# Performance work log

Measured on AMD Instinct MI355X. Metric: run time of the kernel, lower is better.

The kernel has to match this reference:

```python
import jax, jax.numpy as jnp
import numpy as np

HEADS = 8
DIM_HEAD = 64
NUM_LANDMARKS = 256
PINV_ITERS = 6
SCALE = DIM_HEAD ** -0.5
KERNEL = 33
PAD = KERNEL // 2


def moore_penrose_iter_pinv(x, iters=PINV_ITERS):
    # x: [b, h, m, m]
    abs_x = jnp.abs(x)
    col = abs_x.sum(axis=-1)
    row = abs_x.sum(axis=-2)
    # global max over all batch/head entries, as in the torch code
    z = jnp.swapaxes(x, -1, -2) / (jnp.max(col) * jnp.max(row))
    I = jnp.eye(x.shape[-1], dtype=x.dtype)
    for _ in range(iters):
        xz = x @ z
        z = 0.25 * z @ (13.0 * I - xz @ (15.0 * I - xz @ (7.0 * I - xz)))
    return z


def setup_inputs() -> dict:
    key = jax.random.key(0)
    k1, k2, k3, k4 = jax.random.split(key, 4)
    b, n, dim = 4, 4096, 512
    inner = HEADS * DIM_HEAD
    return {
        "x": jax.random.normal(k1, (b, n, dim), dtype=jnp.float32),
        "w_qkv": jax.random.normal(k2, (dim, 3 * inner), dtype=jnp.float32) * 0.02,
        "w_out": jax.random.normal(k3, (inner, dim), dtype=jnp.float32) * 0.02,
        "b_out": jnp.zeros((dim,), dtype=jnp.float32),
        "conv_w": jax.random.normal(k4, (HEADS, 1, KERNEL, 1), dtype=jnp.float32) * 0.1,
    }


def reference(x, w_qkv, w_out, b_out, conv_w):
    b, n, dim = x.shape
    h, m = HEADS, NUM_LANDMARKS
    # n is a multiple of m, so the original's left-padding branch is a no-op
    qkv = x @ w_qkv  # [b, n, 3*h*d]
    q, k, v = jnp.split(qkv, 3, axis=-1)

    def split_heads(t):
        return t.reshape(b, n, h, DIM_HEAD).transpose(0, 2, 1, 3)  # [b,h,n,d]

    q, k, v = split_heads(q), split_heads(k), split_heads(v)
    q = q * SCALE

    l = n // m  # landmark group size
    q_l = q.reshape(b, h, m, l, DIM_HEAD).mean(axis=3)  # [b,h,m,d]
    k_l = k.reshape(b, h, m, l, DIM_HEAD).mean(axis=3)

    sim1 = jnp.einsum("bhid,bhjd->bhij", q, k_l)   # [b,h,n,m]
    sim2 = jnp.einsum("bhid,bhjd->bhij", q_l, k_l)  # [b,h,m,m]
    sim3 = jnp.einsum("bhid,bhjd->bhij", q_l, k)   # [b,h,m,n]

    attn1 = jax.nn.softmax(sim1, axis=-1)
    attn2 = jax.nn.softmax(sim2, axis=-1)
    attn3 = jax.nn.softmax(sim3, axis=-1)

    attn2_inv = moore_penrose_iter_pinv(attn2, PINV_ITERS)
    out = attn1 @ (attn2_inv @ (attn3 @ v))  # [b,h,n,d]

    # residual depthwise conv along sequence dim (kernel 33x1, groups=heads)
    res = jax.lax.conv_general_dilated(
        v, conv_w,
        window_strides=(1, 1),
        padding=((PAD, PAD), (0, 0)),
        dimension_numbers=("NCHW", "OIHW", "NCHW"),
        feature_group_count=h,
    )
    out = out + res

    out = out.transpose(0, 2, 1, 3).reshape(b, n, h * DIM_HEAD)
    out = out @ w_out + b_out
    return out  # out[:, -n:] is identity since no padding was applied
```

## Files before the change

### kernel.cpp

```cpp
#include <hip/hip_runtime.h>
#include <math.h>


#define QKV_STRIDE 262144
#define LM_STRIDE 16384
#define MM_STRIDE 65536

typedef float f32x4 __attribute__((ext_vector_type(4)));
typedef short bf8 __attribute__((ext_vector_type(8)));
typedef short s4v __attribute__((ext_vector_type(4)));

__device__ __forceinline__ unsigned short f2bf_(float f) {
  unsigned u = __float_as_uint(f);
  u += 0x7FFFu + ((u >> 16) & 1u);
  return (unsigned short)(u >> 16);
}
__device__ __forceinline__ float bf2f_(unsigned short h) {
  return __uint_as_float(((unsigned)h) << 16);
}

__device__ __forceinline__ void gl16(const short* g, short* l) {
  __builtin_amdgcn_global_load_lds(
      (const __attribute__((address_space(1))) unsigned int*)g,
      (__attribute__((address_space(3))) unsigned int*)l, 16, 0, 0);
}

__global__ __launch_bounds__(256) void zero_scal(float* scal) {
  if (threadIdx.x < 2) scal[threadIdx.x] = 0.0f;
}

__global__ __launch_bounds__(256) void x_to_bf16(const float* __restrict__ x,
                                                 short* __restrict__ xb) {
  const int g = blockIdx.x * 256 + threadIdx.x;
  const float4* xp = (const float4*)x;
#pragma unroll
  for (int u = 0; u < 4; ++u) {
    const size_t i4 = (size_t)u * 524288 + g;
    float4 v = xp[i4];
    s4v o;
    o[0] = (short)f2bf_(v.x); o[1] = (short)f2bf_(v.y);
    o[2] = (short)f2bf_(v.z); o[3] = (short)f2bf_(v.w);
    *(s4v*)&xb[i4 * 4] = o;
  }
}

__global__ __launch_bounds__(256) void transpose_bf16(const float* __restrict__ src,
                                                      short* __restrict__ dst,
                                                      int R, int C) {
  __shared__ float T[32][33];
  const int t = threadIdx.x;
  const int c0 = blockIdx.x * 32, r0 = blockIdx.y * 32;
  const int tr = t >> 3, tc = (t & 7) << 2;
  float4 vsrc = *(const float4*)&src[(size_t)(r0 + tr) * C + c0 + tc];
  T[tr][tc + 0] = vsrc.x; T[tr][tc + 1] = vsrc.y;
  T[tr][tc + 2] = vsrc.z; T[tr][tc + 3] = vsrc.w;
  __syncthreads();
  s4v o;
  o[0] = (short)f2bf_(T[tc + 0][tr]);
  o[1] = (short)f2bf_(T[tc + 1][tr]);
  o[2] = (short)f2bf_(T[tc + 2][tr]);
  o[3] = (short)f2bf_(T[tc + 3][tr]);
  *(s4v*)&dst[(size_t)(c0 + tr) * R + r0 + tc] = o;
}

__global__ __launch_bounds__(256) void gemm_qkv_mfma(const short* __restrict__ xb,
                                                     const short* __restrict__ wT,
                                                     short* __restrict__ qb16,
                                                     short* __restrict__ kb16,
                                                     short* __restrict__ vT16) {
  __shared__ short SMEM[17408];
  short* As = SMEM;
  short* Bs = SMEM + 4096;
  const int tid = threadIdx.x;
  const int lane = tid & 63, w = tid >> 6;
  const int wr = w >> 1, wc = w & 1;
  const int bid = (blockIdx.x & 7) * 192 + (blockIdx.x >> 3);
  const int bn = bid % 12, bm = bid / 12;
  const int gm0 = bm * 128, gn0 = bn * 128;
  const int mA0 = (tid >> 6) * 16 + (tid & 15), kA0 = ((tid >> 4) & 3) * 8;
  const int s1 = tid + 256;
  const int mA1 = (s1 >> 6) * 16 + (s1 & 15), kA1 = ((s1 >> 4) & 3) * 8;
  const short* srcA0 = &xb[(size_t)(gm0 + mA0) * 512 + kA0];
  const short* srcA1 = &xb[(size_t)(gm0 + mA1) * 512 + kA1];
  const short* srcB0 = &wT[(size_t)(gn0 + mA0) * 512 + kA0];
  const short* srcB1 = &wT[(size_t)(gn0 + mA1) * 512 + kA1];
  short* dA0 = &As[w * 512];
  short* dA1 = &As[2048 + w * 512];
  short* dB0 = &Bs[w * 512];
  short* dB1 = &Bs[2048 + w * 512];
  f32x4 acc[4][4];
#pragma unroll
  for (int i = 0; i < 4; ++i)
#pragma unroll
    for (int j = 0; j < 4; ++j) acc[i][j] = (f32x4){0.f, 0.f, 0.f, 0.f};
  for (int kt = 0; kt < 16; ++kt) {
    const int k0 = kt * 32;
    __syncthreads();
    gl16(srcA0 + k0, dA0);
    gl16(srcA1 + k0, dA1);
    gl16(srcB0 + k0, dB0);
    gl16(srcB1 + k0, dB1);
    __syncthreads();
    bf8 af[4], bf[4];
#pragma unroll
    for (int i = 0; i < 4; ++i) {
      af[i] = *(const bf8*)&As[((wr * 4 + i) * 64 + lane) * 8];
      bf[i] = *(const bf8*)&Bs[((wc * 4 + i) * 64 + lane) * 8];
    }
#pragma unroll
    for (int i = 0; i < 4; ++i)
#pragma unroll
      for (int j = 0; j < 4; ++j)
        acc[i][j] = __builtin_amdgcn_mfma_f32_16x16x32_bf16(af[i], bf[j], acc[i][j], 0, 0, 0);
  }
  const int which = bn >> 2;
  const int qd = lane >> 4, c = lane & 15;
  if (which < 2) {
    short* dst = which == 0 ? qb16 : kb16;
    const float scale = which == 0 ? 0.125f : 1.0f;
#pragma unroll
    for (int i = 0; i < 4; ++i)
#pragma unroll
      for (int j = 0; j < 4; ++j) {
        const int col = gn0 + wc * 64 + j * 16 + c;
        const int head = (col >> 6) & 7, dd = col & 63;
#pragma unroll
        for (int r = 0; r < 4; ++r) {
          const int row = gm0 + wr * 64 + i * 16 + qd * 4 + r;
          const int b = row >> 12, seq = row & 4095;
          dst[(size_t)(b * 8 + head) * QKV_STRIDE + seq * 64 + dd] =
              (short)f2bf_(acc[i][j][r] * scale);
        }
      }
  } else {
    __syncthreads();
#pragma unroll
    for (int i = 0; i < 4; ++i)
#pragma unroll
      for (int j = 0; j < 4; ++j) {
        const int colL = wc * 64 + j * 16 + c;
#pragma unroll
        for (int r = 0; r < 4; ++r) {
          const int rowL = wr * 64 + i * 16 + qd * 4 + r;
          SMEM[colL * 136 + rowL] = (short)f2bf_(acc[i][j][r]);
        }
      }
    __syncthreads();
    const int b = gm0 >> 12, seq0 = gm0 & 4095;
    const int dcol = tid >> 1, half = tid & 1;
    const int col = gn0 + dcol;
    const int head = (col >> 6) & 7, d = col & 63;
    const short* src = &SMEM[dcol * 136 + half * 64];
    short* dstp = &vT16[(size_t)(b * 8 + head) * QKV_STRIDE + (size_t)d * 4096 +
                        seq0 + half * 64];
#pragma unroll
    for (int u = 0; u < 16; ++u) *(s4v*)&dstp[u * 4] = *(const s4v*)&src[u * 4];
  }
}

__global__ __launch_bounds__(256) void lmk_mean(const short* __restrict__ qb16,
                                                const short* __restrict__ kb16,
                                                float* __restrict__ ql,
                                                float* __restrict__ kl,
                                                short* __restrict__ klb16) {
  const int g = blockIdx.x * 256 + threadIdx.x;
  const int dd = g & 63, mi = (g >> 6) & 255, bh = g >> 14;
  const size_t base = (size_t)bh * QKV_STRIDE + mi * 1024 + dd;
  float sq = 0.f, sk = 0.f;
#pragma unroll
  for (int jj = 0; jj < 16; ++jj) {
    sq += bf2f_((unsigned short)qb16[base + jj * 64]);
    sk += bf2f_((unsigned short)kb16[base + jj * 64]);
  }
  const float qv = sq * 0.0625f, kv = sk * 0.0625f;
  ql[g] = qv;
  kl[g] = kv;
  klb16[g] = (short)f2bf_(kv);
}

__global__ __launch_bounds__(256) void sim2_softmax(const float* __restrict__ ql,
                                                    const float* __restrict__ kl,
                                                    short* __restrict__ x2hi,
                                                    short* __restrict__ x2lo) {
  const int blk = blockIdx.x;
  const int bh = blk >> 4, rg = blk & 15;
  __shared__ float Qs[16][64];
  __shared__ float Ks[64][68];
  __shared__ float S[16][257];
  __shared__ float red[16][17];
  __shared__ float rowinv[16];
  const int tid = threadIdx.x;
  const int r = tid >> 4, jc = tid & 15;
#pragma unroll
  for (int u = 0; u < 4; ++u) {
    int t2 = tid + u * 256;
    Qs[t2 >> 6][t2 & 63] =
        ql[(size_t)bh * LM_STRIDE + (rg * 16 + (t2 >> 6)) * 64 + (t2 & 63)];
  }
  for (int c = 0; c < 4; ++c) {
    __syncthreads();
#pragma unroll
    for (int u = 0; u < 4; ++u) {
      int t4 = tid + u * 256;
      int row = t4 >> 4, c4 = (t4 & 15) << 2;
      *(float4*)&Ks[row][c4] =
          *(const float4*)&kl[(size_t)bh * LM_STRIDE + (c * 64 + row) * 64 + c4];
    }
    __syncthreads();
#pragma unroll
    for (int s = 0; s < 4; ++s) {
      const int jj = jc + (s << 4);
      float acc = 0.f;
#pragma unroll
      for (int k4 = 0; k4 < 16; ++k4) {
        const float4 a = *(const float4*)&Qs[r][k4 << 2];
        const float4 bb = *(const float4*)&Ks[jj][k4 << 2];
        acc += a.x * bb.x + a.y * bb.y + a.z * bb.z + a.w * bb.w;
      }
      S[r][(c << 6) + jj] = acc;
    }
  }
  __syncthreads();
  float pm = -3.0e38f;
#pragma unroll
  for (int u = 0; u < 16; ++u) pm = fmaxf(pm, S[r][jc + (u << 4)]);
  red[r][jc] = pm;
  __syncthreads();
  float m = red[r][0];
#pragma unroll
  for (int u = 1; u < 16; ++u) m = fmaxf(m, red[r][u]);
  __syncthreads();
  float ps = 0.f;
#pragma unroll
  for (int u = 0; u < 16; ++u) {
    const int j = jc + (u << 4);
    const float e = __expf(S[r][j] - m);
    S[r][j] = e;
    ps += e;
  }
  red[r][jc] = ps;
  __syncthreads();
  if (jc == 0) {
    float sum = 0.f;
#pragma unroll
    for (int u = 0; u < 16; ++u) sum += red[r][u];
    rowinv[r] = 1.0f / sum;
  }
  __syncthreads();
  for (int idx = tid; idx < 4096; idx += 256) {
    const int rr = idx >> 8, j = idx & 255;
    const float v = S[rr][j] * rowinv[rr];
    const unsigned short h = f2bf_(v);
    const size_t off = (size_t)bh * MM_STRIDE + (rg * 16 + rr) * 256 + j;
    x2hi[off] = (short)h;
    x2lo[off] = (short)f2bf_(v - bf2f_(h));
  }
}

__global__ __launch_bounds__(256) void colrow_max(const short* __restrict__ x2hi,
                                                  const short* __restrict__ x2lo,
                                                  float* __restrict__ scal) {
  const int bh = blockIdx.x;
  const int tid = threadIdx.x;
  const size_t b0 = (size_t)bh * MM_STRIDE;
  float cs = 0.f, rs = 0.f;
  for (int j = 0; j < 256; ++j) {
    const size_t o = b0 + (size_t)tid * 256 + j;
    cs += fabsf(bf2f_((unsigned short)x2hi[o]) + bf2f_((unsigned short)x2lo[o]));
  }
  for (int i = 0; i < 256; ++i) {
    const size_t o = b0 + (size_t)i * 256 + tid;
    rs += fabsf(bf2f_((unsigned short)x2hi[o]) + bf2f_((unsigned short)x2lo[o]));
  }
  __shared__ float rc[256], rr[256];
  rc[tid] = cs; rr[tid] = rs;
  __syncthreads();
  for (int st = 128; st > 0; st >>= 1) {
    if (tid < st) {
      rc[tid] = fmaxf(rc[tid], rc[tid + st]);
      rr[tid] = fmaxf(rr[tid], rr[tid + st]);
    }
    __syncthreads();
  }
  if (tid == 0) {
    atomicMax((int*)&scal[0], __float_as_int(rc[0]));
    atomicMax((int*)&scal[1], __float_as_int(rr[0]));
  }
}

__global__ __launch_bounds__(256) void tscale2(const short* __restrict__ x2hi,
                                               const short* __restrict__ x2lo,
                                               const float* __restrict__ scal,
                                               short* __restrict__ zBhi,
                                               short* __restrict__ zBlo,
                                               short* __restrict__ zAhi,
                                               short* __restrict__ zAlo,
                                               float* __restrict__ zf) {
  const int g = blockIdx.x * 256 + threadIdx.x;
  const int j = g & 255, i = (g >> 8) & 255, bh = g >> 16;
  const float inv = 1.0f / (scal[0] * scal[1]);
  const float val = (bf2f_((unsigned short)x2hi[g]) +
                     bf2f_((unsigned short)x2lo[g])) * inv;
  const unsigned short h = f2bf_(val);
  const unsigned short lo = f2bf_(val - bf2f_(h));
  zBhi[g] = (short)h;
  zBlo[g] = (short)lo;
  const size_t tg = (size_t)bh * MM_STRIDE + (size_t)j * 256 + i;
  zAhi[tg] = (short)h;
  zAlo[tg] = (short)lo;
  zf[tg] = val;
}

__global__ __launch_bounds__(256) void pinv_mfma(const short* __restrict__ Ahi_g,
                                                 const short* __restrict__ Alo_g,
                                                 const short* __restrict__ Bhi_g,
                                                 const short* __restrict__ Blo_g,
                                                 const float* __restrict__ Ef,
                                                 float* __restrict__ Cf,
                                                 short* __restrict__ Chi,
                                                 short* __restrict__ Clo,
                                                 short* __restrict__ CThi,
                                                 short* __restrict__ CTlo,
                                                 float alpha, float beta,
                                                 int wantCf, int wantChl,
                                                 int wantT) {
  __shared__ short Ah[2048], Al[2048], Bh[2048], Bl[2048];
  __shared__ float Tbuf[64 * 68];
  const int tid = threadIdx.x;
  const int lane = tid & 63, w = tid >> 6;
  const int bid = blockIdx.x;
  const int xcd = bid & 7, y = bid >> 3;
  const int t16 = y & 15, bgrp = y >> 4;
  const int batch = bgrp * 8 + xcd;
  const int tm = t16 >> 2, tn = t16 & 3;
  const size_t bb = (size_t)batch * MM_STRIDE;
  const int ml = (tid >> 6) * 16 + (tid & 15), koff = ((tid >> 4) & 3) * 8;
  const short* sAh = Ahi_g + bb + (size_t)(tm * 64 + ml) * 256 + koff;
  const short* sAl = Alo_g + bb + (size_t)(tm * 64 + ml) * 256 + koff;
  const short* sBh = Bhi_g + bb + (size_t)(tn * 64 + ml) * 256 + koff;
  const short* sBl = Blo_g + bb + (size_t)(tn * 64 + ml) * 256 + koff;
  short* dAh = &Ah[w * 512];
  short* dAl = &Al[w * 512];
  short* dBh = &Bh[w * 512];
  short* dBl = &Bl[w * 512];
  f32x4 acc[4];
#pragma unroll
  for (int j = 0; j < 4; ++j) acc[j] = (f32x4){0.f, 0.f, 0.f, 0.f};
  for (int kt = 0; kt < 8; ++kt) {
    const int k0 = kt * 32;
    __syncthreads();
    gl16(sAh + k0, dAh);
    gl16(sAl + k0, dAl);
    gl16(sBh + k0, dBh);
    gl16(sBl + k0, dBl);
    __syncthreads();
    bf8 ah = *(const bf8*)&Ah[(w * 64 + lane) * 8];
    bf8 al = *(const bf8*)&Al[(w * 64 + lane) * 8];
#pragma unroll
    for (int j = 0; j < 4; ++j) {
      bf8 bh = *(const bf8*)&Bh[(j * 64 + lane) * 8];
      bf8 bl = *(const bf8*)&Bl[(j * 64 + lane) * 8];
      acc[j] = __builtin_amdgcn_mfma_f32_16x16x32_bf16(ah, bh, acc[j], 0, 0, 0);
      acc[j] = __builtin_amdgcn_mfma_f32_16x16x32_bf16(ah, bl, acc[j], 0, 0, 0);
      acc[j] = __builtin_amdgcn_mfma_f32_16x16x32_bf16(al, bh, acc[j], 0, 0, 0);
    }
  }
  const int qd = lane >> 4, c = lane & 15;
  float vals[4][4];
#pragma unroll
  for (int j = 0; j < 4; ++j) {
    const int col = tn * 64 + j * 16 + c;
#pragma unroll
    for (int r = 0; r < 4; ++r) {
      const int row = tm * 64 + w * 16 + qd * 4 + r;
      const size_t off = bb + (size_t)row * 256 + col;
      float e = 0.f;
      if (alpha != 0.0f) e = alpha * Ef[off];
      const float vv = e + beta * acc[j][r];
      vals[j][r] = vv;
      if (wantCf) Cf[off] = vv;
      if (wantChl) {
        const unsigned short h = f2bf_(vv);
        Chi[off] = (short)h;
        Clo[off] = (short)f2bf_(vv - bf2f_(h));
      }
    }
  }
  if (wantT) {
    __syncthreads();
#pragma unroll
    for (int j = 0; j < 4; ++j)
#pragma unroll
      for (int r = 0; r < 4; ++r)
        Tbuf[(j * 16 + c) * 68 + w * 16 + qd * 4 + r] = vals[j][r];
    __syncthreads();
    const int ctr = tid >> 2, seg = (tid & 3) * 16;
#pragma unroll
    for (int u = 0; u < 4; ++u) {
      float4 o = *(const float4*)&Tbuf[ctr * 68 + seg + u * 4];
      s4v hi, lo;
      unsigned short h;
      h = f2bf_(o.x); hi[0] = (short)h; lo[0] = (short)f2bf_(o.x - bf2f_(h));
      h = f2bf_(o.y); hi[1] = (short)h; lo[1] = (short)f2bf_(o.y - bf2f_(h));
      h = f2bf_(o.z); hi[2] = (short)h; lo[2] = (short)f2bf_(o.z - bf2f_(h));
      h = f2bf_(o.w); hi[3] = (short)h; lo[3] = (short)f2bf_(o.w - bf2f_(h));
      const size_t off = bb + (size_t)(tn * 64 + ctr) * 256 + tm * 64 + seg + u * 4;
      *(s4v*)&CThi[off] = hi;
      *(s4v*)&CTlo[off] = lo;
    }
  }
}

__global__ __launch_bounds__(256) void attn3_flash(const float* __restrict__ ql,
                                                   const short* __restrict__ kb16,
                                                   const short* __restrict__ vT16,
                                                   float* __restrict__ opart,
                                                   float* __restrict__ mpart,
                                                   float* __restrict__ lpart) {
  const int kc = blockIdx.x;
  const int rt = blockIdx.y;
  const int bh = blockIdx.z;
  __shared__ short Pa[4][4096];
  const int tid = threadIdx.x, lane = tid & 63, w = tid >> 6;
  const int qd = lane >> 4, c = lane & 15;
  const int rw = rt * 64 + w * 16;
  const float* qlp = ql + (size_t)bh * LM_STRIDE;
  const short* kp = kb16 + (size_t)bh * QKV_STRIDE;
  const short* vp = vT16 + (size_t)bh * QKV_STRIDE;
  short* Pw = &Pa[w][0];
  bf8 af[2];
#pragma unroll
  for (int st = 0; st < 2; ++st) {
    float4 x0 = *(const float4*)&qlp[(size_t)(rw + c) * 64 + st * 32 + qd * 8];
    float4 x1 = *(const float4*)&qlp[(size_t)(rw + c) * 64 + st * 32 + qd * 8 + 4];
    bf8 r;
    r[0] = (short)f2bf_(x0.x); r[1] = (short)f2bf_(x0.y);
    r[2] = (short)f2bf_(x0.z); r[3] = (short)f2bf_(x0.w);
    r[4] = (short)f2bf_(x1.x); r[5] = (short)f2bf_(x1.y);
    r[6] = (short)f2bf_(x1.z); r[7] = (short)f2bf_(x1.w);
    af[st] = r;
  }
  float m[4], l[4];
#pragma unroll
  for (int r = 0; r < 4; ++r) { m[r] = -3.0e38f; l[r] = 0.f; }
  f32x4 accO[4];
#pragma unroll
  for (int nb = 0; nb < 4; ++nb) accO[nb] = (f32x4){0.f, 0.f, 0.f, 0.f};
  for (int it = 0; it < 4; ++it) {
    const int kb0 = kc * 1024 + it * 256;
    f32x4 acc[16];
#pragma unroll
    for (int j = 0; j < 16; ++j) acc[j] = (f32x4){0.f, 0.f, 0.f, 0.f};
#pragma unroll
    for (int st = 0; st < 2; ++st)
#pragma unroll
      for (int j = 0; j < 16; ++j) {
        bf8 bfk = *(const bf8*)&kp[(size_t)(kb0 + j * 16 + c) * 64 + st * 32 + qd * 8];
        acc[j] = __builtin_amdgcn_mfma_f32_16x16x32_bf16(af[st], bfk, acc[j], 0, 0, 0);
      }
#pragma unroll
    for (int r = 0; r < 4; ++r) {
      float mx = acc[0][r];
#pragma unroll
      for (int j = 1; j < 16; ++j) mx = fmaxf(mx, acc[j][r]);
      mx = fmaxf(mx, __shfl_xor(mx, 1));
      mx = fmaxf(mx, __shfl_xor(mx, 2));
      mx = fmaxf(mx, __shfl_xor(mx, 4));
      mx = fmaxf(mx, __shfl_xor(mx, 8));
      const float mN = fmaxf(m[r], mx);
      const float a = __expf(m[r] - mN);
      m[r] = mN;
      l[r] *= a;
#pragma unroll
      for (int nb = 0; nb < 4; ++nb) accO[nb][r] *= a;
      float s = 0.f;
#pragma unroll
      for (int j = 0; j < 16; ++j) {
        const float e = __expf(acc[j][r] - mN);
        acc[j][r] = e;
        s += e;
      }
      s += __shfl_xor(s, 1);
      s += __shfl_xor(s, 2);
      s += __shfl_xor(s, 4);
      s += __shfl_xor(s, 8);
      l[r] += s;
    }
#pragma unroll
    for (int j = 0; j < 16; ++j) {
      const int kcol = j * 16 + c;
      const int kb8 = kcol >> 5;
      const int la_base = 16 * ((kcol >> 3) & 3);
      const int j8 = kcol & 7;
#pragma unroll
      for (int r = 0; r < 4; ++r) {
        const int rl = qd * 4 + r;
        Pw[(kb8 * 64 + la_base + rl) * 8 + j8] = (short)f2bf_(acc[j][r]);
      }
    }
#pragma unroll
    for (int kbk = 0; kbk < 8; ++kbk) {
      bf8 ap = *(const bf8*)&Pw[(kbk * 64 + lane) * 8];
#pragma unroll
      for (int nb = 0; nb < 4; ++nb) {
        bf8 bv = *(const bf8*)&vp[(size_t)(nb * 16 + c) * 4096 + kb0 + kbk * 32 + qd * 8];
        accO[nb] = __builtin_amdgcn_mfma_f32_16x16x32_bf16(ap, bv, accO[nb], 0, 0, 0);
      }
    }
  }
  const size_t ob = ((size_t)kc * 32 + bh) * 256 + rt * 64;
#pragma unroll
  for (int nb = 0; nb < 4; ++nb)
#pragma unroll
    for (int r = 0; r < 4; ++r)
      opart[(ob + w * 16 + qd * 4 + r) * 64 + nb * 16 + c] = accO[nb][r];
  if (c == 0) {
#pragma unroll
    for (int r = 0; r < 4; ++r) {
      mpart[ob + w * 16 + qd * 4 + r] = m[r];
      lpart[ob + w * 16 + qd * 4 + r] = l[r];
    }
  }
}

__global__ __launch_bounds__(256) void attn3_merge(const float* __restrict__ opart,
                                                   const float* __restrict__ mpart,
                                                   const float* __restrict__ lpart,
                                                   short* __restrict__ avth,
                                                   short* __restrict__ avtl) {
  const int g = blockIdx.x * 256 + threadIdx.x;
  const int d = g & 63;
  const int idx = g >> 6;
  const int bh = idx >> 8, row = idx & 255;
  const float m0 = mpart[idx], m1 = mpart[8192 + idx],
              m2 = mpart[16384 + idx], m3 = mpart[24576 + idx];
  const float mx = fmaxf(fmaxf(m0, m1), fmaxf(m2, m3));
  const float w0 = __expf(m0 - mx), w1 = __expf(m1 - mx),
              w2 = __expf(m2 - mx), w3 = __expf(m3 - mx);
  const float l = lpart[idx] * w0 + lpart[8192 + idx] * w1 +
                  lpart[16384 + idx] * w2 + lpart[24576 + idx] * w3;
  const float o = opart[(size_t)idx * 64 + d] * w0 +
                  opart[524288 + (size_t)idx * 64 + d] * w1 +
                  opart[1048576 + (size_t)idx * 64 + d] * w2 +
                  opart[1572864 + (size_t)idx * 64 + d] * w3;
  const float val = o / l;
  const unsigned short h = f2bf_(val);
  const size_t o2 = ((size_t)bh * 64 + d) * 256 + row;
  avth[o2] = (short)h;
  avtl[o2] = (short)f2bf_(val - bf2f_(h));
}

__global__ __launch_bounds__(256) void zav_mfma(const short* __restrict__ zAhi,
                                                const short* __restrict__ zAlo,
                                                const short* __restrict__ avth,
                                                const short* __restrict__ avtl,
                                                short* __restrict__ w2tb16) {
  __shared__ short Tb[64 * 68];
  const int rt = blockIdx.x;
  const int bh = blockIdx.y;
  const int tid = threadIdx.x, lane = tid & 63, w = tid >> 6;
  const int qd = lane >> 4, c = lane & 15;
  const size_t zoff = (size_t)bh * MM_STRIDE + (size_t)(rt * 64 + w * 16 + c) * 256;
  const short* zh = zAhi + zoff;
  const short* zl = zAlo + zoff;
  const short* ahp = avth + (size_t)bh * LM_STRIDE;
  const short* alp = avtl + (size_t)bh * LM_STRIDE;
  f32x4 acc[4];
#pragma unroll
  for (int j = 0; j < 4; ++j) acc[j] = (f32x4){0.f, 0.f, 0.f, 0.f};
  for (int kt = 0; kt < 8; ++kt) {
    const int k0 = kt * 32 + qd * 8;
    bf8 ah = *(const bf8*)&zh[k0];
    bf8 al = *(const bf8*)&zl[k0];
#pragma unroll
    for (int j = 0; j < 4; ++j) {
      bf8 bhj = *(const bf8*)&ahp[(size_t)(j * 16 + c) * 256 + k0];
      bf8 blj = *(const bf8*)&alp[(size_t)(j * 16 + c) * 256 + k0];
      acc[j] = __builtin_amdgcn_mfma_f32_16x16x32_bf16(ah, bhj, acc[j], 0, 0, 0);
      acc[j] = __builtin_amdgcn_mfma_f32_16x16x32_bf16(ah, blj, acc[j], 0, 0, 0);
      acc[j] = __builtin_amdgcn_mfma_f32_16x16x32_bf16(al, bhj, acc[j], 0, 0, 0);
    }
  }
#pragma unroll
  for (int j = 0; j < 4; ++j)
#pragma unroll
    for (int r = 0; r < 4; ++r)
      Tb[(j * 16 + c) * 68 + w * 16 + qd * 4 + r] = (short)f2bf_(acc[j][r]);
  __syncthreads();
  const int col = tid >> 2, rs = (tid & 3) * 16;
  short* dst = &w2tb16[(size_t)bh * LM_STRIDE + (size_t)col * 256 + rt * 64 + rs];
  const short* srcp = &Tb[col * 68 + rs];
#pragma unroll
  for (int u = 0; u < 4; ++u) *(s4v*)&dst[u * 4] = *(const s4v*)&srcp[u * 4];
}

__global__ __launch_bounds__(256) void attn1_conv_mfma(const short* __restrict__ qb16,
                                                       const short* __restrict__ klb16,
                                                       const short* __restrict__ w2tb16,
                                                       const short* __restrict__ vT16,
                                                       const float* __restrict__ cw,
                                                       short* __restrict__ ohb16) {
  __shared__ short Pa[16384];
  __shared__ float redM[4][64], redS[4][64];
  __shared__ float rowM[64], rowI[64];
  __shared__ float cwS[33];
  const int tid = threadIdx.x;
  const int lane = tid & 63, w = tid >> 6;
  const int qd = lane >> 4, c = lane & 15;
  const int r0 = blockIdx.x * 64;
  const int bh = blockIdx.y;
  const short* qp = qb16 + (size_t)bh * QKV_STRIDE;
  const short* klp = klb16 + (size_t)bh * LM_STRIDE;
  const short* w2p = w2tb16 + (size_t)bh * LM_STRIDE;
  const short* vp = vT16 + (size_t)bh * QKV_STRIDE;

  if (tid < 33) cwS[tid] = cw[(bh & 7) * 33 + tid];

  f32x4 acc[4][4];
#pragma unroll
  for (int i = 0; i < 4; ++i)
#pragma unroll
    for (int j = 0; j < 4; ++j) acc[i][j] = (f32x4){0.f, 0.f, 0.f, 0.f};
#pragma unroll
  for (int st = 0; st < 2; ++st) {
    const int k0 = st * 32 + qd * 8;
    bf8 af[4], bf[4];
#pragma unroll
    for (int i = 0; i < 4; ++i) {
      af[i] = *(const bf8*)&qp[(size_t)(r0 + i * 16 + c) * 64 + k0];
      bf[i] = *(const bf8*)&klp[(size_t)(w * 64 + i * 16 + c) * 64 + k0];
    }
#pragma unroll
    for (int i = 0; i < 4; ++i)
#pragma unroll
      for (int j = 0; j < 4; ++j)
        acc[i][j] = __builtin_amdgcn_mfma_f32_16x16x32_bf16(af[i], bf[j], acc[i][j], 0, 0, 0);
  }
#pragma unroll
  for (int i = 0; i < 4; ++i)
#pragma unroll
    for (int r = 0; r < 4; ++r) {
      float m0 = fmaxf(fmaxf(acc[i][0][r], acc[i][1][r]),
                       fmaxf(acc[i][2][r], acc[i][3][r]));
      m0 = fmaxf(m0, __shfl_xor(m0, 1));
      m0 = fmaxf(m0, __shfl_xor(m0, 2));
      m0 = fmaxf(m0, __shfl_xor(m0, 4));
      m0 = fmaxf(m0, __shfl_xor(m0, 8));
      if (c == 0) redM[w][i * 16 + qd * 4 + r] = m0;
    }
  __syncthreads();
  if (tid < 64)
    rowM[tid] = fmaxf(fmaxf(redM[0][tid], redM[1][tid]),
                      fmaxf(redM[2][tid], redM[3][tid]));
  __syncthreads();
#pragma unroll
  for (int i = 0; i < 4; ++i)
#pragma unroll
    for (int r = 0; r < 4; ++r) {
      const float mrow = rowM[i * 16 + qd * 4 + r];
      float s = 0.f;
#pragma unroll
      for (int j = 0; j < 4; ++j) {
        const float e = __expf(acc[i][j][r] - mrow);
        acc[i][j][r] = e;
        s += e;
      }
      s += __shfl_xor(s, 1);
      s += __shfl_xor(s, 2);
      s += __shfl_xor(s, 4);
      s += __shfl_xor(s, 8);
      if (c == 0) redS[w][i * 16 + qd * 4 + r] = s;
    }
  __syncthreads();
  if (tid < 64)
    rowI[tid] = 1.0f / (redS[0][tid] + redS[1][tid] + redS[2][tid] + redS[3][tid]);
  __syncthreads();
#pragma unroll
  for (int i = 0; i < 4; ++i)
#pragma unroll
    for (int r = 0; r < 4; ++r) {
      const int row = i * 16 + qd * 4 + r;
      const float inv = rowI[row];
#pragma unroll
      for (int j = 0; j < 4; ++j) {
        const int col = w * 64 + j * 16 + c;
        const short val = (short)f2bf_(acc[i][j][r] * inv);
        const int kb = col >> 5;
        const int lane2 = (row & 15) + 16 * ((col >> 3) & 3);
        Pa[((kb * 4 + i) * 64 + lane2) * 8 + (col & 7)] = val;
      }
    }
  __syncthreads();
  f32x4 accO[4];
#pragma unroll
  for (int nb = 0; nb < 4; ++nb) accO[nb] = (f32x4){0.f, 0.f, 0.f, 0.f};
  for (int kb = 0; kb < 8; ++kb) {
    bf8 ap = *(const bf8*)&Pa[((kb * 4 + w) * 64 + lane) * 8];
#pragma unroll
    for (int nb = 0; nb < 4; ++nb) {
      bf8 bfr = *(const bf8*)&w2p[(size_t)(nb * 16 + c) * 256 + kb * 32 + qd * 8];
      accO[nb] = __builtin_amdgcn_mfma_f32_16x16x32_bf16(ap, bfr, accO[nb], 0, 0, 0);
    }
  }
  {
    bf8 ba[3];
    const int rl = w * 16 + (lane & 15);
#pragma unroll
    for (int kb = 0; kb < 3; ++kb) {
#pragma unroll
      for (int e = 0; e < 8; ++e) {
        const int kk = kb * 32 + qd * 8 + e;
        const int t = kk - rl;
        const int s = r0 - 16 + kk;
        const float bv = (t >= 0 && t < 33 && s >= 0 && s < 4096) ? cwS[t] : 0.f;
        ba[kb][e] = (short)f2bf_(bv);
      }
    }
#pragma unroll
    for (int kb = 0; kb < 3; ++kb) {
      int s0 = r0 - 16 + kb * 32 + qd * 8;
      s0 = s0 < 0 ? 0 : (s0 > 4088 ? 4088 : s0);
#pragma unroll
      for (int nb = 0; nb < 4; ++nb) {
        bf8 bv = *(const bf8*)&vp[(size_t)(nb * 16 + c) * 4096 + s0];
        accO[nb] = __builtin_amdgcn_mfma_f32_16x16x32_bf16(ba[kb], bv, accO[nb], 0, 0, 0);
      }
    }
  }
  short* ohp = (short*)ohb16 + (size_t)bh * QKV_STRIDE;
#pragma unroll
  for (int nb = 0; nb < 4; ++nb)
#pragma unroll
    for (int r = 0; r < 4; ++r) {
      const int row = r0 + w * 16 + qd * 4 + r;
      ohp[(size_t)row * 64 + nb * 16 + c] = (short)f2bf_(accO[nb][r]);
    }
}

__global__ __launch_bounds__(256) void gemm_out_mfma(const short* __restrict__ ohb16,
                                                     const short* __restrict__ wT,
                                                     const float* __restrict__ bias,
                                                     float* __restrict__ out) {
  __shared__ short As[4096];
  __shared__ short Bs[4096];
  const int tid = threadIdx.x;
  const int lane = tid & 63, w = tid >> 6;
  const int wr = w >> 1, wc = w & 1;
  const int bid = (blockIdx.x & 7) * 64 + (blockIdx.x >> 3);
  const int bn = bid & 3, bm = bid >> 2;
  const int gm0 = bm * 128, gn0 = bn * 128;
  const int mA0 = (tid >> 6) * 16 + (tid & 15), kA0 = ((tid >> 4) & 3) * 8;
  const int s1 = tid + 256;
  const int mA1 = (s1 >> 6) * 16 + (s1 & 15), kA1 = ((s1 >> 4) & 3) * 8;
  const int b0r = (gm0 + mA0) >> 12, seq0 = (gm0 + mA0) & 4095;
  const int b1r = (gm0 + mA1) >> 12, seq1 = (gm0 + mA1) & 4095;
  short* dA0 = &As[w * 512];
  short* dA1 = &As[2048 + w * 512];
  short* dB0 = &Bs[w * 512];
  short* dB1 = &Bs[2048 + w * 512];
  f32x4 acc[4][4];
#pragma unroll
  for (int i = 0; i < 4; ++i)
#pragma unroll
    for (int j = 0; j < 4; ++j) acc[i][j] = (f32x4){0.f, 0.f, 0.f, 0.f};
  for (int kt = 0; kt < 16; ++kt) {
    const int ka = kt * 32 + kA0, kb = kt * 32 + kA1;
    __syncthreads();
    gl16(&ohb16[(size_t)(b0r * 8 + (ka >> 6)) * QKV_STRIDE + (size_t)seq0 * 64 + (ka & 63)], dA0);
    gl16(&ohb16[(size_t)(b1r * 8 + (kb >> 6)) * QKV_STRIDE + (size_t)seq1 * 64 + (kb & 63)], dA1);
    gl16(&wT[(size_t)(gn0 + mA0) * 512 + ka], dB0);
    gl16(&wT[(size_t)(gn0 + mA1) * 512 + kb], dB1);
    __syncthreads();
    bf8 af[4], bfr[4];
#pragma unroll
    for (int i = 0; i < 4; ++i) {
      af[i] = *(const bf8*)&As[((wr * 4 + i) * 64 + lane) * 8];
      bfr[i] = *(const bf8*)&Bs[((wc * 4 + i) * 64 + lane) * 8];
    }
#pragma unroll
    for (int i = 0; i < 4; ++i)
#pragma unroll
      for (int j = 0; j < 4; ++j)
        acc[i][j] = __builtin_amdgcn_mfma_f32_16x16x32_bf16(af[i], bfr[j], acc[i][j], 0, 0, 0);
  }
  const int qd = lane >> 4, c = lane & 15;
#pragma unroll
  for (int i = 0; i < 4; ++i)
#pragma unroll
    for (int j = 0; j < 4; ++j) {
      const int col = gn0 + wc * 64 + j * 16 + c;
      const float bval = bias[col];
#pragma unroll
      for (int r = 0; r < 4; ++r) {
        const int row = gm0 + wr * 64 + i * 16 + qd * 4 + r;
        out[(size_t)row * 512 + col] = acc[i][j][r] + bval;
      }
    }
}

extern "C" void kernel_launch(void* const* d_in, const int* in_sizes, int n_in,
                              void* d_out, int out_size, void* d_ws, size_t ws_size,
                              hipStream_t stream) {
  const float* x    = (const float*)d_in[0];
  const float* wqkv = (const float*)d_in[1];
  const float* wout = (const float*)d_in[2];
  const float* bout = (const float*)d_in[3];
  const float* cw   = (const float*)d_in[4];
  float* out = (float*)d_out;

  float* w = (float*)d_ws;
  short* qb16   = (short*)(w);
  short* kb16   = (short*)(w + 4194304);
  short* vT16   = (short*)(w + 8388608);
  short* xb16   = (short*)(w + 12582912);
  float* z0f    = w + 12582912;
  float* z1f    = w + 14680064;
  float* opart  = w + 12582912;
  short* ohb16  = (short*)(w + 12582912);
  float* ql     = w + 16777216;
  float* kl     = w + 17301504;
  short* klb16  = (short*)(w + 17825792);
  short* x2hi   = (short*)(w + 18087936);
  short* x2lo   = (short*)(w + 19136512);
  float* xzf    = w + 20185088;
  short* xzAhi  = (short*)(w + 22282240);
  short* xzAlo  = (short*)(w + 23330816);
  short* xzBhi  = (short*)(w + 24379392);
  short* xzBlo  = (short*)(w + 25427968);
  short* u1Bhi  = (short*)(w + 26476544);
  short* u1Blo  = (short*)(w + 27525120);
  short* z0Ahi  = (short*)(w + 28573696);
  short* z0Alo  = (short*)(w + 29622272);
  short* z0Bhi  = (short*)(w + 30670848);
  short* z0Blo  = (short*)(w + 31719424);
  short* z1Ahi  = (short*)(w + 32768000);
  short* z1Alo  = (short*)(w + 33816576);
  short* z1Bhi  = (short*)(w + 34865152);
  short* z1Blo  = (short*)(w + 35913728);
  float* scal   = w + 36962304;
  short* wqkvT  = (short*)(w + 36962368);
  short* woutT  = (short*)(w + 37355584);
  short* avth   = (short*)(w + 20185088);
  short* avtl   = (short*)(w + 20447232);
  short* w2tb16 = (short*)(w + 20709376);
  float* mpart  = w + 26476544;
  float* lpart  = w + 26509312;

  zero_scal<<<1, 64, 0, stream>>>(scal);
  transpose_bf16<<<dim3(48, 16), 256, 0, stream>>>(wqkv, wqkvT, 512, 1536);
  transpose_bf16<<<dim3(16, 16), 256, 0, stream>>>(wout, woutT, 512, 512);
  x_to_bf16<<<2048, 256, 0, stream>>>(x, xb16);
  gemm_qkv_mfma<<<1536, 256, 0, stream>>>(xb16, wqkvT, qb16, kb16, vT16);
  lmk_mean<<<2048, 256, 0, stream>>>(qb16, kb16, ql, kl, klb16);
  sim2_softmax<<<512, 256, 0, stream>>>(ql, kl, x2hi, x2lo);
  colrow_max<<<32, 256, 0, stream>>>(x2hi, x2lo, scal);
  tscale2<<<8192, 256, 0, stream>>>(x2hi, x2lo, scal, z0Bhi, z0Blo, z0Ahi, z0Alo, z0f);

  float *zcf = z0f, *znf = z1f;
  short *zAh = z0Ahi, *zAl = z0Alo, *zBh = z0Bhi, *zBl = z0Blo;
  short *nAh = z1Ahi, *nAl = z1Alo, *nBh = z1Bhi, *nBl = z1Blo;
  for (int it = 0; it < 6; ++it) {
    pinv_mfma<<<512, 256, 0, stream>>>(x2hi, x2lo, zBh, zBl, xzf,
                                       xzf, xzAhi, xzAlo, xzBhi, xzBlo,
                                       0.f, 1.f, 1, 1, 1);
    pinv_mfma<<<512, 256, 0, stream>>>(xzAhi, xzAlo, xzBhi, xzBlo, xzf,
                                       znf, u1Bhi, u1Blo, u1Bhi, u1Blo,
                                       7.f, -1.f, 0, 0, 1);
    pinv_mfma<<<512, 256, 0, stream>>>(xzAhi, xzAlo, u1Bhi, u1Blo, xzf,
                                       znf, xzBhi, xzBlo, xzBhi, xzBlo,
                                       15.f, -1.f, 0, 0, 1);
    pinv_mfma<<<512, 256, 0, stream>>>(zAh, zAl, xzBhi, xzBlo, zcf,
                                       znf, nAh, nAl, nBh, nBl,
                                       3.25f, -0.25f, 1, 1, 1);
    float* tf = zcf; zcf = znf; znf = tf;
    short* t;
    t = zAh; zAh = nAh; nAh = t;  t = zAl; zAl = nAl; nAl = t;
    t = zBh; zBh = nBh; nBh = t;  t = zBl; zBl = nBl; nBl = t;
  }

  attn3_flash<<<dim3(4, 4, 32), 256, 0, stream>>>(ql, kb16, vT16, opart, mpart, lpart);
  attn3_merge<<<2048, 256, 0, stream>>>(opart, mpart, lpart, avth, avtl);
  zav_mfma<<<dim3(4, 32), 256, 0, stream>>>(zAh, zAl, avth, avtl, w2tb16);
  attn1_conv_mfma<<<dim3(64, 32), 256, 0, stream>>>(qb16, klb16, w2tb16, vT16, cw, ohb16);
  gemm_out_mfma<<<512, 256, 0, stream>>>(ohb16, woutT, bout, out);
}
```

Before: 801.4 us.

## Give each wave full softmax rows in attn1 kernel, remap blocks to XCDs, skip unused pinv outputs

```diff
diff --git a/kernel.cpp b/kernel.cpp
--- a/kernel.cpp
+++ b/kernel.cpp
@@ -137,7 +137,7 @@
 #pragma unroll
     for (int i = 0; i < 4; ++i)
 #pragma unroll
-      for (int j = 0; j < 4; ++j) {
+    for (int j = 0; j < 4; ++j) {
         const int colL = wc * 64 + j * 16 + c;
 #pragma unroll
         for (int r = 0; r < 4; ++r) {
@@ -600,125 +600,101 @@
                                                        const short* __restrict__ vT16,
                                                        const float* __restrict__ cw,
                                                        short* __restrict__ ohb16) {
-  __shared__ short Pa[16384];
-  __shared__ float redM[4][64], redS[4][64];
-  __shared__ float rowM[64], rowI[64];
+  __shared__ short Pa[4][4096];
   __shared__ float cwS[33];
-  const int tid = threadIdx.x;
-  const int lane = tid & 63, w = tid >> 6;
+  const int tid = threadIdx.x, lane = tid & 63, w = tid >> 6;
   const int qd = lane >> 4, c = lane & 15;
-  const int r0 = blockIdx.x * 64;
-  const int bh = blockIdx.y;
+  const int lin = blockIdx.x;
+  const int xcd = lin & 7;
+  const int idx = lin >> 3;
+  const int bh = xcd * 4 + (idx >> 6);
+  const int r0 = (idx & 63) * 64;
+  const int rw = r0 + w * 16;
   const short* qp = qb16 + (size_t)bh * QKV_STRIDE;
   const short* klp = klb16 + (size_t)bh * LM_STRIDE;
   const short* w2p = w2tb16 + (size_t)bh * LM_STRIDE;
   const short* vp = vT16 + (size_t)bh * QKV_STRIDE;
-
-  if (tid < 33) cwS[tid] = cw[(bh & 7) * 33 + tid];
-
-  f32x4 acc[4][4];
-#pragma unroll
-  for (int i = 0; i < 4; ++i)
-#pragma unroll
-    for (int j = 0; j < 4; ++j) acc[i][j] = (f32x4){0.f, 0.f, 0.f, 0.f};
-#pragma unroll
-  for (int st = 0; st < 2; ++st) {
-    const int k0 = st * 32 + qd * 8;
-    bf8 af[4], bf[4];
-#pragma unroll
-    for (int i = 0; i < 4; ++i) {
-      af[i] = *(const bf8*)&qp[(size_t)(r0 + i * 16 + c) * 64 + k0];
-      bf[i] = *(const bf8*)&klp[(size_t)(w * 64 + i * 16 + c) * 64 + k0];
-    }
-#pragma unroll
-    for (int i = 0; i < 4; ++i)
-#pragma unroll
-      for (int j = 0; j < 4; ++j)
-        acc[i][j] = __builtin_amdgcn_mfma_f32_16x16x32_bf16(af[i], bf[j], acc[i][j], 0, 0, 0);
-  }
-#pragma unroll
-  for (int i = 0; i < 4; ++i)
+  short* Pw = &Pa[w][0];
+  if (lane < 33) cwS[lane] = cw[(bh & 7) * 33 + lane];
+  bf8 af[2];
+#pragma unroll
+  for (int st = 0; st < 2; ++st)
+    af[st] = *(const bf8*)&qp[(size_t)(rw + c) * 64 + st * 32 + qd * 8];
+  f32x4 acc[16];
+#pragma unroll
+  for (int j = 0; j < 16; ++j) acc[j] = (f32x4){0.f, 0.f, 0.f, 0.f};
+#pragma unroll
+  for (int st = 0; st < 2; ++st)
+#pragma unroll
+    for (int j = 0; j < 16; ++j) {
+      bf8 bfk = *(const bf8*)&klp[(size_t)(j * 16 + c) * 64 + st * 32 + qd * 8];
+      acc[j] = __builtin_amdgcn_mfma_f32_16x16x32_bf16(af[st], bfk, acc[j], 0, 0, 0);
+    }
+#pragma unroll
+  for (int r = 0; r < 4; ++r) {
+    float mx = acc[0][r];
+#pragma unroll
+    for (int j = 1; j < 16; ++j) mx = fmaxf(mx, acc[j][r]);
+    mx = fmaxf(mx, __shfl_xor(mx, 1));
+    mx = fmaxf(mx, __shfl_xor(mx, 2));
+    mx = fmaxf(mx, __shfl_xor(mx, 4));
+    mx = fmaxf(mx, __shfl_xor(mx, 8));
+    float s = 0.f;
+#pragma unroll
+    for (int j = 0; j < 16; ++j) {
+      const float e = __expf(acc[j][r] - mx);
+      acc[j][r] = e;
+      s += e;
+    }
+    s += __shfl_xor(s, 1);
+    s += __shfl_xor(s, 2);
+    s += __shfl_xor(s, 4);
+    s += __shfl_xor(s, 8);
+    const float inv = 1.0f / s;
+#pragma unroll
+    for (int j = 0; j < 16; ++j) acc[j][r] *= inv;
+  }
+#pragma unroll
+  for (int j = 0; j < 16; ++j) {
+    const int kcol = j * 16 + c;
+    const int kb8 = kcol >> 5;
+    const int la_base = 16 * ((kcol >> 3) & 3);
+    const int j8 = kcol & 7;
 #pragma unroll
     for (int r = 0; r < 4; ++r) {
-      float m0 = fmaxf(fmaxf(acc[i][0][r], acc[i][1][r]),
-                       fmaxf(acc[i][2][r], acc[i][3][r]));
-      m0 = fmaxf(m0, __shfl_xor(m0, 1));
-      m0 = fmaxf(m0, __shfl_xor(m0, 2));
-      m0 = fmaxf(m0, __shfl_xor(m0, 4));
-      m0 = fmaxf(m0, __shfl_xor(m0, 8));
-      if (c == 0) redM[w][i * 16 + qd * 4 + r] = m0;
-    }
-  __syncthreads();
-  if (tid < 64)
-    rowM[tid] = fmaxf(fmaxf(redM[0][tid], redM[1][tid]),
-                      fmaxf(redM[2][tid], redM[3][tid]));
-  __syncthreads();
-#pragma unroll
-  for (int i = 0; i < 4; ++i)
-#pragma unroll
-    for (int r = 0; r < 4; ++r) {
-      const float mrow = rowM[i * 16 + qd * 4 + r];
-      float s = 0.f;
-#pragma unroll
-      for (int j = 0; j < 4; ++j) {
-        const float e = __expf(acc[i][j][r] - mrow);
-        acc[i][j][r] = e;
-        s += e;
-      }
-      s += __shfl_xor(s, 1);
-      s += __shfl_xor(s, 2);
-      s += __shfl_xor(s, 4);
-      s += __shfl_xor(s, 8);
-      if (c == 0) redS[w][i * 16 + qd * 4 + r] = s;
-    }
-  __syncthreads();
-  if (tid < 64)
-    rowI[tid] = 1.0f / (redS[0][tid] + redS[1][tid] + redS[2][tid] + redS[3][tid]);
-  __syncthreads();
-#pragma unroll
-  for (int i = 0; i < 4; ++i)
-#pragma unroll
-    for (int r = 0; r < 4; ++r) {
-      const int row = i * 16 + qd * 4 + r;
-      const float inv = rowI[row];
-#pragma unroll
-      for (int j = 0; j < 4; ++j) {
-        const int col = w * 64 + j * 16 + c;
-        const short val = (short)f2bf_(acc[i][j][r] * inv);
-        const int kb = col >> 5;
-        const int lane2 = (row & 15) + 16 * ((col >> 3) & 3);
-        Pa[((kb * 4 + i) * 64 + lane2) * 8 + (col & 7)] = val;
-      }
-    }
-  __syncthreads();
+      const int rl = qd * 4 + r;
+      Pw[(kb8 * 64 + la_base + rl) * 8 + j8] = (short)f2bf_(acc[j][r]);
+    }
+  }
   f32x4 accO[4];
 #pragma unroll
   for (int nb = 0; nb < 4; ++nb) accO[nb] = (f32x4){0.f, 0.f, 0.f, 0.f};
-  for (int kb = 0; kb < 8; ++kb) {
-    bf8 ap = *(const bf8*)&Pa[((kb * 4 + w) * 64 + lane) * 8];
+#pragma unroll
+  for (int kbk = 0; kbk < 8; ++kbk) {
+    bf8 ap = *(const bf8*)&Pw[(kbk * 64 + lane) * 8];
 #pragma unroll
     for (int nb = 0; nb < 4; ++nb) {
-      bf8 bfr = *(const bf8*)&w2p[(size_t)(nb * 16 + c) * 256 + kb * 32 + qd * 8];
-      accO[nb] = __builtin_amdgcn_mfma_f32_16x16x32_bf16(ap, bfr, accO[nb], 0, 0, 0);
+      bf8 bv = *(const bf8*)&w2p[(size_t)(nb * 16 + c) * 256 + kbk * 32 + qd * 8];
+      accO[nb] = __builtin_amdgcn_mfma_f32_16x16x32_bf16(ap, bv, accO[nb], 0, 0, 0);
     }
   }
   {
-    bf8 ba[3];
-    const int rl = w * 16 + (lane & 15);
-#pragma unroll
-    for (int kb = 0; kb < 3; ++kb) {
+    bf8 ba[2];
+    const int rl = lane & 15;
+#pragma unroll
+    for (int kb = 0; kb < 2; ++kb) {
 #pragma unroll
       for (int e = 0; e < 8; ++e) {
         const int kk = kb * 32 + qd * 8 + e;
         const int t = kk - rl;
-        const int s = r0 - 16 + kk;
+        const int s = rw - 16 + kk;
         const float bv = (t >= 0 && t < 33 && s >= 0 && s < 4096) ? cwS[t] : 0.f;
         ba[kb][e] = (short)f2bf_(bv);
       }
     }
 #pragma unroll
-    for (int kb = 0; kb < 3; ++kb) {
-      int s0 = r0 - 16 + kb * 32 + qd * 8;
+    for (int kb = 0; kb < 2; ++kb) {
+      int s0 = rw - 16 + kb * 32 + qd * 8;
       s0 = s0 < 0 ? 0 : (s0 > 4088 ? 4088 : s0);
 #pragma unroll
       for (int nb = 0; nb < 4; ++nb) {
@@ -732,7 +708,7 @@
   for (int nb = 0; nb < 4; ++nb)
 #pragma unroll
     for (int r = 0; r < 4; ++r) {
-      const int row = r0 + w * 16 + qd * 4 + r;
+      const int row = rw + qd * 4 + r;
       ohp[(size_t)row * 64 + nb * 16 + c] = (short)f2bf_(accO[nb][r]);
     }
 }
@@ -860,6 +836,7 @@
   short *zAh = z0Ahi, *zAl = z0Alo, *zBh = z0Bhi, *zBl = z0Blo;
   short *nAh = z1Ahi, *nAl = z1Alo, *nBh = z1Bhi, *nBl = z1Blo;
   for (int it = 0; it < 6; ++it) {
+    const int nl = (it < 5) ? 1 : 0;
     pinv_mfma<<<512, 256, 0, stream>>>(x2hi, x2lo, zBh, zBl, xzf,
                                        xzf, xzAhi, xzAlo, xzBhi, xzBlo,
                                        0.f, 1.f, 1, 1, 1);
@@ -871,7 +848,7 @@
                                        15.f, -1.f, 0, 0, 1);
     pinv_mfma<<<512, 256, 0, stream>>>(zAh, zAl, xzBhi, xzBlo, zcf,
                                        znf, nAh, nAl, nBh, nBl,
-                                       3.25f, -0.25f, 1, 1, 1);
+                                       3.25f, -0.25f, nl, 1, nl);
     float* tf = zcf; zcf = znf; znf = tf;
     short* t;
     t = zAh; zAh = nAh; nAh = t;  t = zAl; zAl = nAl; nAl = t;
@@ -881,6 +858,6 @@
   attn3_flash<<<dim3(4, 4, 32), 256, 0, stream>>>(ql, kb16, vT16, opart, mpart, lpart);
   attn3_merge<<<2048, 256, 0, stream>>>(opart, mpart, lpart, avth, avtl);
   zav_mfma<<<dim3(4, 32), 256, 0, stream>>>(zAh, zAl, avth, avtl, w2tb16);
-  attn1_conv_mfma<<<dim3(64, 32), 256, 0, stream>>>(qb16, klb16, w2tb16, vT16, cw, ohb16);
+  attn1_conv_mfma<<<2048, 256, 0, stream>>>(qb16, klb16, w2tb16, vT16, cw, ohb16);
   gemm_out_mfma<<<512, 256, 0, stream>>>(ohb16, woutT, bout, out);
 }
```

New measurement: 788.2 us. No clear change (-1.6%).
